# Performance work log

Hardware: AMD Instinct MI355X
Metric: run time of the kernel (lower is better)

The kernel has to match this reference:

```python
import jax, jax.numpy as jnp
import numpy as np

N, DIM, E = 2048, 16, 65536


def setup_inputs() -> dict:
    key = jax.random.key(0)
    k1, k2, k3, k4 = jax.random.split(key, 4)
    emb_nodes = jax.random.normal(k1, (N, DIM), dtype=jnp.float32)
    edge_list = jax.random.randint(k2, (2, E), 0, N, dtype=jnp.int32)
    # nn.Linear(2*dim, 1): weight [1, 2*dim], bias [1]
    bound = 1.0 / np.sqrt(2 * DIM)
    W = jax.random.uniform(k3, (1, 2 * DIM), minval=-bound, maxval=bound, dtype=jnp.float32)
    b = jax.random.uniform(k4, (1,), minval=-bound, maxval=bound, dtype=jnp.float32)
    return {"emb_nodes": emb_nodes, "edge_list": edge_list, "W": W, "b": b}


def reference(emb_nodes, edge_list, W, b):
    n, d = emb_nodes.shape
    # torch code detaches the pairwise embeddings -> stop_gradient here
    e = jax.lax.stop_gradient(emb_nodes)
    # pair p = i*n + j : first node i, second node j
    interleaved = jnp.repeat(e, n, axis=0)          # [n*n, d] = e[i]
    repeated = jnp.tile(e, (n, 1))                  # [n*n, d] = e[j]
    edge_embeddings = jnp.concatenate([interleaved, repeated], axis=1)  # [n*n, 2d]
    # self-loop mask: |e[i]-e[j]| sums to 0 (i.e. identical embeddings)
    non_empty_mask = jnp.abs(interleaved - repeated).sum(axis=1) > 0    # [n*n] bool
    edge_logits = edge_embeddings @ W.T + b         # [n*n, 1]
    logits_without_self_loops = jnp.where(non_empty_mask, edge_logits[:, 0], -10.0)
    # vectorized membership: pair (i,j) is a true edge iff it appears in edge_list
    # (embeddings drawn from a continuous dist are distinct a.s., so equality of
    # concatenated embeddings <=> equality of (i,j) index pairs)
    flat_idx = edge_list[0].astype(jnp.int32) * n + edge_list[1].astype(jnp.int32)
    true_edges = jnp.zeros((n * n,), dtype=jnp.float32).at[flat_idx].set(1.0)
    return edge_embeddings, logits_without_self_loops, true_edges
```

## Files before the change

kernel.cpp:

```cpp
#include <hip/hip_runtime.h>

constexpr int NN   = 2048;
constexpr int DIMM = 16;
constexpr int NE   = 65536;

__global__ void node_dots_kernel(const float* __restrict__ emb,
                                 const float* __restrict__ W,
                                 float* __restrict__ ac) {
    int i = blockIdx.x * blockDim.x + threadIdx.x;
    if (i >= NN) return;
    const float4* row = reinterpret_cast<const float4*>(emb) + i * 4;
    const float4* w   = reinterpret_cast<const float4*>(W);
    float a = 0.f, c = 0.f;
#pragma unroll
    for (int k = 0; k < 4; ++k) {
        float4 r  = row[k];
        float4 wl = w[k];
        float4 wh = w[k + 4];
        a += r.x * wl.x + r.y * wl.y + r.z * wl.z + r.w * wl.w;
        c += r.x * wh.x + r.y * wh.y + r.z * wh.z + r.w * wh.w;
    }
    ac[i]      = a;
    ac[NN + i] = c;
}

__global__ void emb_pairs_kernel(const float4* __restrict__ emb4,
                                 float4* __restrict__ out4, int total_q) {
    int stride = gridDim.x * blockDim.x;
    for (int q = blockIdx.x * blockDim.x + threadIdx.x; q < total_q; q += stride) {
        int p  = q >> 3;
        int c4 = q & 7;
        int i  = p >> 11;
        int j  = p & (NN - 1);
        int row = (c4 < 4) ? i : j;
        out4[q] = emb4[row * 4 + (c4 & 3)];
    }
}

template <bool USE_WS>
__global__ void logits_kernel(const float* __restrict__ emb,
                              const float* __restrict__ W,
                              const float* __restrict__ bptr,
                              const float* __restrict__ ac,
                              float4* __restrict__ logits4,
                              float4* __restrict__ true4, int total4) {
    int stride = gridDim.x * blockDim.x;
    float bb = bptr[0];
    for (int t = blockIdx.x * blockDim.x + threadIdx.x; t < total4; t += stride) {
        int p0 = t << 2;
        int i  = p0 >> 11;
        int j0 = p0 & (NN - 1);
        float a;
        float4 cv;
        if constexpr (USE_WS) {
            a  = ac[i];
            cv = *reinterpret_cast<const float4*>(ac + NN + j0);
        } else {
            const float4* w  = reinterpret_cast<const float4*>(W);
            const float4* ri = reinterpret_cast<const float4*>(emb) + i * 4;
            a = 0.f;
#pragma unroll
            for (int k = 0; k < 4; ++k) {
                float4 r = ri[k], wl = w[k];
                a += r.x * wl.x + r.y * wl.y + r.z * wl.z + r.w * wl.w;
            }
            float cvals[4];
#pragma unroll
            for (int jj = 0; jj < 4; ++jj) {
                const float4* rj = reinterpret_cast<const float4*>(emb) + (j0 + jj) * 4;
                float s = 0.f;
#pragma unroll
                for (int k = 0; k < 4; ++k) {
                    float4 r = rj[k], wh = w[k + 4];
                    s += r.x * wh.x + r.y * wh.y + r.z * wh.z + r.w * wh.w;
                }
                cvals[jj] = s;
            }
            cv = make_float4(cvals[0], cvals[1], cvals[2], cvals[3]);
        }
        float base = a + bb;
        float4 o;
        o.x = (j0 + 0 == i) ? -10.0f : base + cv.x;
        o.y = (j0 + 1 == i) ? -10.0f : base + cv.y;
        o.z = (j0 + 2 == i) ? -10.0f : base + cv.z;
        o.w = (j0 + 3 == i) ? -10.0f : base + cv.w;
        logits4[t] = o;
        true4[t]   = make_float4(0.f, 0.f, 0.f, 0.f);
    }
}

__global__ void scatter_kernel(const int* __restrict__ el,
                               float* __restrict__ true_e) {
    int t = blockIdx.x * blockDim.x + threadIdx.x;
    if (t >= NE) return;
    int i = el[t];
    int j = el[NE + t];
    true_e[i * NN + j] = 1.0f;
}

extern "C" void kernel_launch(void* const* d_in, const int* in_sizes, int n_in,
                              void* d_out, int out_size, void* d_ws, size_t ws_size,
                              hipStream_t stream) {
    const float* emb = (const float*)d_in[0];
    const int*   el  = (const int*)d_in[1];
    const float* W   = (const float*)d_in[2];
    const float* b   = (const float*)d_in[3];

    float* out        = (float*)d_out;
    float* out_emb    = out;
    float* out_logits = out + (size_t)NN * NN * 2 * DIMM;
    float* out_true   = out_logits + (size_t)NN * NN;

    const int total_q = NN * NN * 8;
    const int total4  = NN * NN / 4;

    const bool use_ws = ws_size >= (size_t)(2 * NN) * sizeof(float);
    float* ac = (float*)d_ws;

    if (use_ws)
        node_dots_kernel<<<(NN + 255) / 256, 256, 0, stream>>>(emb, W, ac);

    emb_pairs_kernel<<<8192, 256, 0, stream>>>(
        (const float4*)emb, (float4*)out_emb, total_q);

    if (use_ws)
        logits_kernel<true><<<4096, 256, 0, stream>>>(
            emb, W, b, ac, (float4*)out_logits, (float4*)out_true, total4);
    else
        logits_kernel<false><<<4096, 256, 0, stream>>>(
            emb, W, b, nullptr, (float4*)out_logits, (float4*)out_true, total4);

    scatter_kernel<<<(NE + 255) / 256, 256, 0, stream>>>(el, out_true);
}
```

Measured before the change: 567.5 us.

## Fuse pair-embedding and logits streams into one kernel with nontemporal stores

Merges the node-dot, pair-embedding copy and logits/zeroing kernels into a single kernel. The grid is sized so each thread writes exactly one logits float4, and the embedding copy is unrolled eight at a time with all loads issued before the stores. Output writes use nontemporal stores to avoid cache pollution on the roughly 600 MB write stream. Logit dots are recomputed per thread instead of read from workspace, which removes the extra launches and the workspace dependency but adds redundant small loads.

```diff
diff --git a/kernel.cpp b/kernel.cpp
--- a/kernel.cpp
+++ b/kernel.cpp
@@ -1,96 +1,86 @@
 #include <hip/hip_runtime.h>
 
-constexpr int NN   = 2048;
-constexpr int DIMM = 16;
-constexpr int NE   = 65536;
+constexpr int NN = 2048;
+constexpr int NE = 65536;
 
-__global__ void node_dots_kernel(const float* __restrict__ emb,
-                                 const float* __restrict__ W,
-                                 float* __restrict__ ac) {
-    int i = blockIdx.x * blockDim.x + threadIdx.x;
-    if (i >= NN) return;
-    const float4* row = reinterpret_cast<const float4*>(emb) + i * 4;
-    const float4* w   = reinterpret_cast<const float4*>(W);
-    float a = 0.f, c = 0.f;
+constexpr int THREADS       = 256;
+constexpr int BLOCKS        = 4096;
+constexpr int TOTAL_THREADS = THREADS * BLOCKS;
+constexpr int TOTAL_Q       = NN * NN * 8;
+constexpr int ITERS_A       = TOTAL_Q / TOTAL_THREADS;
+constexpr int TOTAL4        = NN * NN / 4;
+
+typedef float f32x4 __attribute__((ext_vector_type(4)));
+
+__global__ __launch_bounds__(256) void fused_streams_kernel(
+    const f32x4* __restrict__ emb4,
+    const float* __restrict__ W,
+    const float* __restrict__ bptr,
+    f32x4* __restrict__ out_emb4,
+    f32x4* __restrict__ logits4,
+    f32x4* __restrict__ true4) {
+    const int tid = blockIdx.x * blockDim.x + threadIdx.x;
+
+    for (int o = 0; o < ITERS_A / 8; ++o) {
+        const int qb = tid + o * 8 * TOTAL_THREADS;
+        f32x4 v[8];
 #pragma unroll
-    for (int k = 0; k < 4; ++k) {
-        float4 r  = row[k];
-        float4 wl = w[k];
-        float4 wh = w[k + 4];
-        a += r.x * wl.x + r.y * wl.y + r.z * wl.z + r.w * wl.w;
-        c += r.x * wh.x + r.y * wh.y + r.z * wh.z + r.w * wh.w;
+        for (int u = 0; u < 8; ++u) {
+            const int q  = qb + u * TOTAL_THREADS;
+            const int p  = q >> 3;
+            const int c4 = q & 7;
+            const int i  = p >> 11;
+            const int j  = p & (NN - 1);
+            const int row = (c4 < 4) ? i : j;
+            v[u] = emb4[row * 4 + (c4 & 3)];
+        }
+#pragma unroll
+        for (int u = 0; u < 8; ++u) {
+            const int q = qb + u * TOTAL_THREADS;
+            __builtin_nontemporal_store(v[u], &out_emb4[q]);
+        }
     }
-    ac[i]      = a;
-    ac[NN + i] = c;
-}
 
-__global__ void emb_pairs_kernel(const float4* __restrict__ emb4,
-                                 float4* __restrict__ out4, int total_q) {
-    int stride = gridDim.x * blockDim.x;
-    for (int q = blockIdx.x * blockDim.x + threadIdx.x; q < total_q; q += stride) {
-        int p  = q >> 3;
-        int c4 = q & 7;
-        int i  = p >> 11;
-        int j  = p & (NN - 1);
-        int row = (c4 < 4) ? i : j;
-        out4[q] = emb4[row * 4 + (c4 & 3)];
+    {
+        const int t  = tid;
+        const int p0 = t << 2;
+        const int i  = p0 >> 11;
+        const int j0 = p0 & (NN - 1);
+
+        const f32x4* w  = reinterpret_cast<const f32x4*>(W);
+        const f32x4* ri = emb4 + i * 4;
+        float a = 0.f;
+#pragma unroll
+        for (int k = 0; k < 4; ++k) {
+            f32x4 r = ri[k], wl = w[k];
+            a += r.x * wl.x + r.y * wl.y + r.z * wl.z + r.w * wl.w;
+        }
+        float cvals[4];
+#pragma unroll
+        for (int jj = 0; jj < 4; ++jj) {
+            const f32x4* rj = emb4 + (j0 + jj) * 4;
+            float s = 0.f;
+#pragma unroll
+            for (int k = 0; k < 4; ++k) {
+                f32x4 r = rj[k], wh = w[k + 4];
+                s += r.x * wh.x + r.y * wh.y + r.z * wh.z + r.w * wh.w;
+            }
+            cvals[jj] = s;
+        }
+        const float base = a + bptr[0];
+        f32x4 o;
+        o.x = (j0 + 0 == i) ? -10.0f : base + cvals[0];
+        o.y = (j0 + 1 == i) ? -10.0f : base + cvals[1];
+        o.z = (j0 + 2 == i) ? -10.0f : base + cvals[2];
+        o.w = (j0 + 3 == i) ? -10.0f : base + cvals[3];
+        __builtin_nontemporal_store(o, &logits4[t]);
+        f32x4 z = {0.f, 0.f, 0.f, 0.f};
+        true4[t] = z;
     }
 }
 
-template <bool USE_WS>
-__global__ void logits_kernel(const float* __restrict__ emb,
-                              const float* __restrict__ W,
-                              const float* __restrict__ bptr,
-                              const float* __restrict__ ac,
-                              float4* __restrict__ logits4,
-                              float4* __restrict__ true4, int total4) {
-    int stride = gridDim.x * blockDim.x;
-    float bb = bptr[0];
-    for (int t = blockIdx.x * blockDim.x + threadIdx.x; t < total4; t += stride) {
-        int p0 = t << 2;
-        int i  = p0 >> 11;
-        int j0 = p0 & (NN - 1);
-        float a;
-        float4 cv;
-        if constexpr (USE_WS) {
-            a  = ac[i];
-            cv = *reinterpret_cast<const float4*>(ac + NN + j0);
-        } else {
-            const float4* w  = reinterpret_cast<const float4*>(W);
-            const float4* ri = reinterpret_cast<const float4*>(emb) + i * 4;
-            a = 0.f;
-#pragma unroll
-            for (int k = 0; k < 4; ++k) {
-                float4 r = ri[k], wl = w[k];
-                a += r.x * wl.x + r.y * wl.y + r.z * wl.z + r.w * wl.w;
-            }
-            float cvals[4];
-#pragma unroll
-            for (int jj = 0; jj < 4; ++jj) {
-                const float4* rj = reinterpret_cast<const float4*>(emb) + (j0 + jj) * 4;
-                float s = 0.f;
-#pragma unroll
-                for (int k = 0; k < 4; ++k) {
-                    float4 r = rj[k], wh = w[k + 4];
-                    s += r.x * wh.x + r.y * wh.y + r.z * wh.z + r.w * wh.w;
-                }
-                cvals[jj] = s;
-            }
-            cv = make_float4(cvals[0], cvals[1], cvals[2], cvals[3]);
-        }
-        float base = a + bb;
-        float4 o;
-        o.x = (j0 + 0 == i) ? -10.0f : base + cv.x;
-        o.y = (j0 + 1 == i) ? -10.0f : base + cv.y;
-        o.z = (j0 + 2 == i) ? -10.0f : base + cv.z;
-        o.w = (j0 + 3 == i) ? -10.0f : base + cv.w;
-        logits4[t] = o;
-        true4[t]   = make_float4(0.f, 0.f, 0.f, 0.f);
-    }
-}
-
-__global__ void scatter_kernel(const int* __restrict__ el,
-                               float* __restrict__ true_e) {
+__global__ __launch_bounds__(256) void scatter_kernel(
+    const int* __restrict__ el, float* __restrict__ true_e) {
     int t = blockIdx.x * blockDim.x + threadIdx.x;
     if (t >= NE) return;
     int i = el[t];
@@ -108,27 +98,12 @@
 
     float* out        = (float*)d_out;
     float* out_emb    = out;
-    float* out_logits = out + (size_t)NN * NN * 2 * DIMM;
+    float* out_logits = out + (size_t)NN * NN * 32;
     float* out_true   = out_logits + (size_t)NN * NN;
 
-    const int total_q = NN * NN * 8;
-    const int total4  = NN * NN / 4;
+    fused_streams_kernel<<<BLOCKS, THREADS, 0, stream>>>(
+        (const f32x4*)emb, W, b,
+        (f32x4*)out_emb, (f32x4*)out_logits, (f32x4*)out_true);
 
-    const bool use_ws = ws_size >= (size_t)(2 * NN) * sizeof(float);
-    float* ac = (float*)d_ws;
-
-    if (use_ws)
-        node_dots_kernel<<<(NN + 255) / 256, 256, 0, stream>>>(emb, W, ac);
-
-    emb_pairs_kernel<<<8192, 256, 0, stream>>>(
-        (const float4*)emb, (float4*)out_emb, total_q);
-
-    if (use_ws)
-        logits_kernel<true><<<4096, 256, 0, stream>>>(
-            emb, W, b, ac, (float4*)out_logits, (float4*)out_true, total4);
-    else
-        logits_kernel<false><<<4096, 256, 0, stream>>>(
-            emb, W, b, nullptr, (float4*)out_logits, (float4*)out_true, total4);
-
-    scatter_kernel<<<(NE + 255) / 256, 256, 0, stream>>>(el, out_true);
+    scatter_kernel<<<(NE + THREADS - 1) / THREADS, THREADS, 0, stream>>>(el, out_true);
 }
```

Measured after the change: 594.6 us. 1.05x slower.
